# Kernel tuning notes

Hardware: AMD Instinct MI355X
Metric: run time of the kernel (lower is better)

## Reference

```python
import jax, jax.numpy as jnp
import numpy as np

B, C, H, W = 4, 256, 64, 64
C8 = C // 8  # q/k projection dim = 32

def setup_inputs() -> dict:
    key = jax.random.key(0)
    ks = jax.random.split(key, 6)
    s = 0.02
    return {
        "x": jax.random.normal(ks[0], (B, C, H, W), dtype=jnp.float32),
        "wq": jax.random.normal(ks[1], (C8, C), dtype=jnp.float32) * s,
        "bq": jnp.zeros((C8,), dtype=jnp.float32),
        "wk": jax.random.normal(ks[2], (C8, C), dtype=jnp.float32) * s,
        "bk": jnp.zeros((C8,), dtype=jnp.float32),
        "wv": jax.random.normal(ks[3], (C, C), dtype=jnp.float32) * s,
        "bv": jnp.zeros((C,), dtype=jnp.float32),
        "wo": jax.random.normal(ks[4], (C, C), dtype=jnp.float32) * s,
        "bo": jnp.zeros((C,), dtype=jnp.float32),
        "scale": jnp.zeros((1,), dtype=jnp.float32),
    }

def reference(x, wq, bq, wk, bk, wv, bv, wo, bo, scale):
    b, c, h, w = x.shape
    n = h * w
    xf = x.reshape(b, c, n)  # (B, C, N)
    # 1x1 convs are channel-mixing GEMMs
    q = jnp.einsum('oc,bcn->bon', wq, xf) + bq[None, :, None]  # (B, C8, N)
    k = jnp.einsum('oc,bcn->bon', wk, xf) + bk[None, :, None]  # (B, C8, N)
    v = jnp.einsum('oc,bcn->bon', wv, xf) + bv[None, :, None]  # (B, C,  N)
    inv_sqrt = 1.0 / jnp.sqrt(jnp.asarray(c // 8, dtype=x.dtype))
    scores = jnp.einsum('bon,bom->bnm', q, k) * inv_sqrt  # (B, N, N): query n, key m
    attn = jax.nn.softmax(scores, axis=-1)
    # torch: bmm(value, attn^T) -> attended[:, :, n] = sum_m v[:, :, m] * attn[n, m]
    attended = jnp.einsum('bcm,bnm->bcn', v, attn)  # (B, C, N)
    out = jnp.einsum('oc,bcn->bon', wo, attended) + bo[None, :, None]
    out = out.reshape(b, c, h, w)
    return x + scale[0] * out
```

## Files before the change

### kernel.cpp

```cpp
#include <hip/hip_runtime.h>
#include <stdint.h>

#define B_ 4
#define C_ 256
#define C8_ 32
#define N_ 4096
#define LOG2E 1.4426950408889634f
#define INV_SQRT32 0.17677669529663689f
#define QSCALE (INV_SQRT32 * LOG2E)

typedef __bf16 bf16x8 __attribute__((ext_vector_type(8)));
typedef float f32x16 __attribute__((ext_vector_type(16)));
typedef unsigned int uint4v __attribute__((ext_vector_type(4)));

__device__ __forceinline__ uint16_t f2bf(float f) {
  uint32_t u = __builtin_bit_cast(uint32_t, f);
  return (uint16_t)((u + 0x7FFFu + ((u >> 16) & 1u)) >> 16);
}
__device__ __forceinline__ uint32_t pack2bf(float a, float b) {
  uint32_t ua = __builtin_bit_cast(uint32_t, a);
  uint32_t ub = __builtin_bit_cast(uint32_t, b);
  ua = (ua + 0x7FFFu + ((ua >> 16) & 1u)) >> 16;
  ub = (ub + 0x7FFFu + ((ub >> 16) & 1u)) & 0xFFFF0000u;
  return ua | ub;
}
__device__ __forceinline__ bf16x8 load_bf8(const uint16_t* p) {
  uint4v u = *(const uint4v*)p;
  return __builtin_bit_cast(bf16x8, u);
}
__device__ __forceinline__ f32x16 mfma32(bf16x8 a, bf16x8 b, f32x16 c) {
  return __builtin_amdgcn_mfma_f32_32x32x16_bf16(a, b, c, 0, 0, 0);
}
__device__ __forceinline__ f32x16 mfma32_f8(long a, long b, f32x16 c) {
  return __builtin_amdgcn_mfma_f32_32x32x16_fp8_fp8(a, b, c, 0, 0, 0);
}
__device__ __forceinline__ long u2l(uint2 u) {
  return (long)(((uint64_t)u.y << 32) | u.x);
}

__global__ void k_wcast(const float* __restrict__ wq, const float* __restrict__ wk,
                        const float* __restrict__ wv, const float* __restrict__ wo,
                        uint16_t* __restrict__ wqb, uint16_t* __restrict__ wkb,
                        uint16_t* __restrict__ wvb, uint16_t* __restrict__ wob) {
  int i = blockIdx.x * 256 + threadIdx.x;
  if (i < 8192) {
    int o = i >> 8, c = i & 255;
    wqb[((size_t)(c >> 3) * 32 + o) * 8 + (c & 7)] = f2bf(wq[i]);
  } else if (i < 16384) {
    int j = i - 8192; int o = j >> 8, c = j & 255;
    wkb[((size_t)(c >> 3) * 32 + o) * 8 + (c & 7)] = f2bf(wk[j]);
  } else if (i < 81920) {
    int j = i - 16384; int o = j >> 8, c = j & 255;
    wvb[((size_t)(c >> 3) * 256 + o) * 8 + (c & 7)] = f2bf(wv[j]);
  } else {
    int j = i - 81920; int o = j >> 8, c = j & 255;
    wob[((size_t)(c >> 3) * 256 + o) * 8 + (c & 7)] = f2bf(wo[j]);
  }
}

__global__ __launch_bounds__(640) void k_proj_qkv(
    const float* __restrict__ x,
    const uint16_t* __restrict__ wqb, const float* __restrict__ bq,
    const uint16_t* __restrict__ wkb, const float* __restrict__ bk,
    const uint16_t* __restrict__ wvb, const float* __restrict__ bv,
    uint16_t* __restrict__ Qb, uint16_t* __restrict__ Kt, uint8_t* __restrict__ V8) {
  __shared__ uint4v xTv[32 * 32];
  int b = blockIdx.y;
  int n0 = blockIdx.x * 32;
  int tid = threadIdx.x;
  uint16_t* xT = (uint16_t*)xTv;

  if (tid < 256) {
    int r = tid >> 3;
    int l4 = (tid & 7) * 4;
#pragma unroll
    for (int p = 0; p < 8; p++) {
      int c = p * 32 + r;
      float4 v = *(const float4*)(x + ((size_t)b * C_ + c) * N_ + n0 + l4);
      int cg = c >> 3, cj = c & 7;
      xT[(cg * 32 + l4 + 0) * 8 + cj] = f2bf(v.x);
      xT[(cg * 32 + l4 + 1) * 8 + cj] = f2bf(v.y);
      xT[(cg * 32 + l4 + 2) * 8 + cj] = f2bf(v.z);
      xT[(cg * 32 + l4 + 3) * 8 + cj] = f2bf(v.w);
    }
  }
  __syncthreads();

  int wave = tid >> 6;
  int lane = tid & 63;
  int h = lane >> 5, ln = lane & 31;

  if (wave == 0) {
    f32x16 aq;
#pragma unroll
    for (int i = 0; i < 16; i++) aq[i] = 0.0f;
#pragma unroll 4
    for (int c = 0; c < C_; c += 16) {
      bf16x8 bb = __builtin_bit_cast(bf16x8, xTv[(c / 8 + h) * 32 + ln]);
      aq = mfma32(load_bf8(wqb + ((size_t)(c / 8 + h) * 32 + ln) * 8), bb, aq);
    }
#pragma unroll
    for (int g = 0; g < 4; g++) {
      int row = g * 8 + h * 4;
      uint2 pq;
      pq.x = pack2bf((aq[4 * g + 0] + bq[row + 0]) * QSCALE,
                     (aq[4 * g + 1] + bq[row + 1]) * QSCALE);
      pq.y = pack2bf((aq[4 * g + 2] + bq[row + 2]) * QSCALE,
                     (aq[4 * g + 3] + bq[row + 3]) * QSCALE);
      *(uint2*)(Qb + ((size_t)b * N_ + n0 + ln) * C8_ + row) = pq;
    }
  } else if (wave == 1) {
    f32x16 ak;
#pragma unroll
    for (int i = 0; i < 16; i++) ak[i] = 0.0f;
#pragma unroll 4
    for (int c = 0; c < C_; c += 16) {
      bf16x8 bb = __builtin_bit_cast(bf16x8, xTv[(c / 8 + h) * 32 + ln]);
      ak = mfma32(load_bf8(wkb + ((size_t)(c / 8 + h) * 32 + ln) * 8), bb, ak);
    }
#pragma unroll
    for (int g = 0; g < 4; g++) {
      int row = g * 8 + h * 4;
      uint2 pk;
      pk.x = pack2bf(ak[4 * g + 0] + bk[row + 0], ak[4 * g + 1] + bk[row + 1]);
      pk.y = pack2bf(ak[4 * g + 2] + bk[row + 2], ak[4 * g + 3] + bk[row + 3]);
      *(uint2*)(Kt + ((size_t)(b * 4 + g) * N_ + n0 + ln) * 8 + h * 4) = pk;
    }
  } else {
    int o0 = (wave - 2) * 32;
    f32x16 a0;
#pragma unroll
    for (int i = 0; i < 16; i++) a0[i] = 0.0f;
#pragma unroll 4
    for (int c = 0; c < C_; c += 16) {
      bf16x8 xa = __builtin_bit_cast(bf16x8, xTv[(c / 8 + h) * 32 + ln]);
      a0 = mfma32(xa, load_bf8(wvb + ((size_t)(c / 8 + h) * 256 + o0 + ln) * 8), a0);
    }
    int och = o0 + ln;
    float b0v = bv[och];
    size_t kgb = (size_t)(b * 512 + (n0 >> 3));
#pragma unroll
    for (int g = 0; g < 4; ++g) {
      uint32_t w0 = __builtin_amdgcn_cvt_pk_fp8_f32(a0[4 * g + 0] + b0v,
                                                    a0[4 * g + 1] + b0v, 0, false);
      w0 = __builtin_amdgcn_cvt_pk_fp8_f32(a0[4 * g + 2] + b0v,
                                           a0[4 * g + 3] + b0v, w0, true);
      *(uint32_t*)(V8 + ((kgb + g) * 256 + och) * 8 + 4 * h) = w0;
    }
  }
}

__global__ __launch_bounds__(512, 4) void k_attn(
    const uint16_t* __restrict__ Qb, const uint16_t* __restrict__ Kt,
    const uint8_t* __restrict__ V8, const uint16_t* __restrict__ Wob,
    const float* __restrict__ bo, const float* __restrict__ x,
    const float* __restrict__ scale, float* __restrict__ out) {
  __shared__ uint32_t Pl[2][2048];
  __shared__ uint4v aTv[32 * 32];
  __shared__ float sl[8][32];

  int bx = blockIdx.x;
  int b = bx >> 1;
  int qt = blockIdx.y + 64 * (bx & 1);
  int wave = threadIdx.x >> 6;
  int lane = threadIdx.x & 63;
  int h = lane >> 5, ln = lane & 31;
  int qi = qt * 32 + ln;

  const uint16_t* qrow = Qb + ((size_t)b * N_ + qi) * C8_;
  bf16x8 qf1 = load_bf8(qrow + h * 8);
  bf16x8 qf2 = load_bf8(qrow + 16 + h * 8);
  const uint16_t* k1base = Kt + ((size_t)(b * 4 + h) * N_) * 8;
  const uint16_t* k2base = Kt + ((size_t)(b * 4 + 2 + h) * N_) * 8;

  int o0 = wave * 32;
  const uint8_t* vbase =
      V8 + (size_t)(b * 512) * 2048 + (size_t)h * 2048 + (size_t)(o0 + ln) * 8;

  f32x16 O;
#pragma unroll
  for (int r = 0; r < 16; r++) O[r] = 0.0f;
  float lsum = 0.0f;

  const int K0 = wave * 32;
  bf16x8 ka1 = load_bf8(k1base + (size_t)(K0 + ln) * 8);
  bf16x8 ka2 = load_bf8(k2base + (size_t)(K0 + ln) * 8);

  for (int c = 0; c < 16; ++c) {
    int kbn = ((c + 1) & 15) * 256 + K0;
    bf16x8 kn1 = load_bf8(k1base + (size_t)(kbn + ln) * 8);
    bf16x8 kn2 = load_bf8(k2base + (size_t)(kbn + ln) * 8);

    f32x16 S;
#pragma unroll
    for (int i = 0; i < 16; i++) S[i] = 0.0f;
    S = mfma32(ka1, qf1, S);
    S = mfma32(ka2, qf2, S);

    float P[16];
#pragma unroll
    for (int r = 0; r < 16; r++) P[r] = __builtin_amdgcn_exp2f(fminf(S[r], 7.5f));
    float l0 = 0.0f, l1 = 0.0f;
#pragma unroll
    for (int r = 0; r < 8; r++) { l0 += P[r]; l1 += P[r + 8]; }
    lsum += l0 + l1;

    uint32_t w0 = __builtin_amdgcn_cvt_pk_fp8_f32(P[0], P[1], 0, false);
    w0 = __builtin_amdgcn_cvt_pk_fp8_f32(P[2], P[3], w0, true);
    uint32_t w1 = __builtin_amdgcn_cvt_pk_fp8_f32(P[4], P[5], 0, false);
    w1 = __builtin_amdgcn_cvt_pk_fp8_f32(P[6], P[7], w1, true);
    uint32_t w2 = __builtin_amdgcn_cvt_pk_fp8_f32(P[8], P[9], 0, false);
    w2 = __builtin_amdgcn_cvt_pk_fp8_f32(P[10], P[11], w2, true);
    uint32_t w3 = __builtin_amdgcn_cvt_pk_fp8_f32(P[12], P[13], 0, false);
    w3 = __builtin_amdgcn_cvt_pk_fp8_f32(P[14], P[15], w3, true);
    uint32_t* pw = &Pl[c & 1][wave * 256 + ln * 2 + h];
    pw[0] = w0; pw[64] = w1; pw[128] = w2; pw[192] = w3;

    __syncthreads();

    const uint8_t* vp = vbase + (size_t)c * 65536;
    const uint32_t* pb = &Pl[c & 1][h * 64 + ln * 2];
    __builtin_amdgcn_s_setprio(1);
#pragma unroll 4
    for (int g = 0; g < 16; ++g) {
      uint2 u1 = *(const uint2*)(vp + (size_t)g * 4096);
      uint2 pu = *(const uint2*)(pb + g * 128);
      O = mfma32_f8(u2l(u1), u2l(pu), O);
    }
    __builtin_amdgcn_s_setprio(0);
    ka1 = kn1; ka2 = kn2;
  }

  lsum += __shfl_xor(lsum, 32, 64);
  if (h == 0) sl[wave][ln] = lsum;
  __syncthreads();
  float lg = 0.0f;
#pragma unroll
  for (int w = 0; w < 8; w++) lg += sl[w][ln];
  float inv = 1.0f / lg;
  uint2* aT2 = (uint2*)aTv;
#pragma unroll
  for (int g = 0; g < 4; ++g) {
    uint2 pr2;
    pr2.x = pack2bf(O[4 * g + 0] * inv, O[4 * g + 1] * inv);
    pr2.y = pack2bf(O[4 * g + 2] * inv, O[4 * g + 3] * inv);
    aT2[((wave * 4 + g) * 32 + ln) * 2 + h] = pr2;
  }
  __syncthreads();

  f32x16 acc;
#pragma unroll
  for (int i = 0; i < 16; i++) acc[i] = 0.0f;
#pragma unroll 4
  for (int cc = 0; cc < C_; cc += 16) {
    bf16x8 a = load_bf8(Wob + ((size_t)(cc / 8 + h) * 256 + o0 + ln) * 8);
    bf16x8 bb = __builtin_bit_cast(bf16x8, aTv[(cc / 8 + h) * 32 + ln]);
    acc = mfma32(a, bb, acc);
  }
  float s = scale[0];
#pragma unroll
  for (int r = 0; r < 16; r++) {
    int row = (r & 3) + 8 * (r >> 2) + 4 * h;
    int o = o0 + row;
    size_t idx = ((size_t)b * C_ + o) * N_ + qi;
    out[idx] = x[idx] + s * (acc[r] + bo[o]);
  }
}

extern "C" void kernel_launch(void* const* d_in, const int* in_sizes, int n_in,
                              void* d_out, int out_size, void* d_ws, size_t ws_size,
                              hipStream_t stream) {
  const float* x  = (const float*)d_in[0];
  const float* wq = (const float*)d_in[1];
  const float* bq = (const float*)d_in[2];
  const float* wk = (const float*)d_in[3];
  const float* bk = (const float*)d_in[4];
  const float* wv = (const float*)d_in[5];
  const float* bv = (const float*)d_in[6];
  const float* wo = (const float*)d_in[7];
  const float* bo = (const float*)d_in[8];
  const float* scale = (const float*)d_in[9];
  float* out = (float*)d_out;

  char* w = (char*)d_ws;
  uint16_t* Qb  = (uint16_t*)(w);
  uint16_t* Kt  = (uint16_t*)(w + (1u << 20));
  uint8_t*  V8  = (uint8_t*)(w + (2u << 20));
  uint16_t* Wqb = (uint16_t*)(w + (6u << 20));
  uint16_t* Wkb = Wqb + 32 * 256;
  uint16_t* Wvb = Wkb + 32 * 256;
  uint16_t* Wob = Wvb + 256 * 256;

  k_wcast<<<576, 256, 0, stream>>>(wq, wk, wv, wo, Wqb, Wkb, Wvb, Wob);
  k_proj_qkv<<<dim3(N_ / 32, B_), 640, 0, stream>>>(x, Wqb, bq, Wkb, bk, Wvb, bv,
                                                    Qb, Kt, V8);
  k_attn<<<dim3(8, 64), 512, 0, stream>>>(Qb, Kt, V8, Wob, bo, x, scale, out);
}
```

Before: 143.8 us.

## Process two query tiles per block and software-pipeline P production with PV MFMA

Each attention block now handles 64 queries as two 32-query tiles, so every fp8 V fragment loaded from global memory feeds two MFMAs and K loads are shared across both tiles. This halves V/K global traffic per query. The loop is also restructured so that the exp/convert of chunk c overlaps the PV MFMA of chunk c-1, which leaves one barrier per iteration. In exchange, register use roughly doubles (launch bounds drop to 2 waves/SIMD), the grid halves to 256 blocks, and LDS use grows.

```diff
diff --git a/kernel.cpp b/kernel.cpp
--- a/kernel.cpp
+++ b/kernel.cpp
@@ -36,6 +36,22 @@
 }
 __device__ __forceinline__ long u2l(uint2 u) {
   return (long)(((uint64_t)u.y << 32) | u.x);
+}
+
+__device__ __forceinline__ float produce_P(const f32x16 S, uint32_t* pw) {
+  float P[16];
+#pragma unroll
+  for (int r = 0; r < 16; r++) P[r] = __builtin_amdgcn_exp2f(fminf(S[r], 7.5f));
+  float l0 = 0.0f, l1 = 0.0f;
+#pragma unroll
+  for (int r = 0; r < 8; r++) { l0 += P[r]; l1 += P[r + 8]; }
+#pragma unroll
+  for (int s = 0; s < 4; ++s) {
+    uint32_t w = __builtin_amdgcn_cvt_pk_fp8_f32(P[4 * s + 0], P[4 * s + 1], 0, false);
+    w = __builtin_amdgcn_cvt_pk_fp8_f32(P[4 * s + 2], P[4 * s + 3], w, true);
+    pw[s * 64] = w;
+  }
+  return l0 + l1;
 }
 
 __global__ void k_wcast(const float* __restrict__ wq, const float* __restrict__ wk,
@@ -150,26 +166,30 @@
   }
 }
 
-__global__ __launch_bounds__(512, 4) void k_attn(
+__global__ __launch_bounds__(512, 2) void k_attn(
     const uint16_t* __restrict__ Qb, const uint16_t* __restrict__ Kt,
     const uint8_t* __restrict__ V8, const uint16_t* __restrict__ Wob,
     const float* __restrict__ bo, const float* __restrict__ x,
     const float* __restrict__ scale, float* __restrict__ out) {
-  __shared__ uint32_t Pl[2][2048];
-  __shared__ uint4v aTv[32 * 32];
-  __shared__ float sl[8][32];
+  __shared__ uint32_t Pl[2][2][2048];
+  __shared__ uint4v aTv[32 * 64];
+  __shared__ float sl[8][2][32];
 
   int bx = blockIdx.x;
   int b = bx >> 1;
-  int qt = blockIdx.y + 64 * (bx & 1);
+  int qt = blockIdx.y + 32 * (bx & 1);
   int wave = threadIdx.x >> 6;
   int lane = threadIdx.x & 63;
   int h = lane >> 5, ln = lane & 31;
-  int qi = qt * 32 + ln;
-
-  const uint16_t* qrow = Qb + ((size_t)b * N_ + qi) * C8_;
-  bf16x8 qf1 = load_bf8(qrow + h * 8);
-  bf16x8 qf2 = load_bf8(qrow + 16 + h * 8);
+  int qiA = qt * 64 + ln;
+  int qiB = qiA + 32;
+
+  const uint16_t* qrowA = Qb + ((size_t)b * N_ + qiA) * C8_;
+  const uint16_t* qrowB = Qb + ((size_t)b * N_ + qiB) * C8_;
+  bf16x8 qf1A = load_bf8(qrowA + h * 8);
+  bf16x8 qf2A = load_bf8(qrowA + 16 + h * 8);
+  bf16x8 qf1B = load_bf8(qrowB + h * 8);
+  bf16x8 qf2B = load_bf8(qrowB + 16 + h * 8);
   const uint16_t* k1base = Kt + ((size_t)(b * 4 + h) * N_) * 8;
   const uint16_t* k2base = Kt + ((size_t)(b * 4 + 2 + h) * N_) * 8;
 
@@ -177,93 +197,124 @@
   const uint8_t* vbase =
       V8 + (size_t)(b * 512) * 2048 + (size_t)h * 2048 + (size_t)(o0 + ln) * 8;
 
-  f32x16 O;
-#pragma unroll
-  for (int r = 0; r < 16; r++) O[r] = 0.0f;
-  float lsum = 0.0f;
+  f32x16 OA, OB;
+#pragma unroll
+  for (int r = 0; r < 16; r++) { OA[r] = 0.0f; OB[r] = 0.0f; }
+  float lsA = 0.0f, lsB = 0.0f;
 
   const int K0 = wave * 32;
   bf16x8 ka1 = load_bf8(k1base + (size_t)(K0 + ln) * 8);
   bf16x8 ka2 = load_bf8(k2base + (size_t)(K0 + ln) * 8);
 
-  for (int c = 0; c < 16; ++c) {
+  {
+    bf16x8 kn1 = load_bf8(k1base + (size_t)(256 + K0 + ln) * 8);
+    bf16x8 kn2 = load_bf8(k2base + (size_t)(256 + K0 + ln) * 8);
+    f32x16 SA, SB;
+#pragma unroll
+    for (int i = 0; i < 16; i++) { SA[i] = 0.0f; SB[i] = 0.0f; }
+    SA = mfma32(ka1, qf1A, SA);
+    SA = mfma32(ka2, qf2A, SA);
+    SB = mfma32(ka1, qf1B, SB);
+    SB = mfma32(ka2, qf2B, SB);
+    lsA += produce_P(SA, &Pl[0][0][wave * 256 + ln * 2 + h]);
+    lsB += produce_P(SB, &Pl[0][1][wave * 256 + ln * 2 + h]);
+    ka1 = kn1; ka2 = kn2;
+  }
+  __syncthreads();
+
+  for (int c = 1; c < 16; ++c) {
     int kbn = ((c + 1) & 15) * 256 + K0;
     bf16x8 kn1 = load_bf8(k1base + (size_t)(kbn + ln) * 8);
     bf16x8 kn2 = load_bf8(k2base + (size_t)(kbn + ln) * 8);
 
-    f32x16 S;
-#pragma unroll
-    for (int i = 0; i < 16; i++) S[i] = 0.0f;
-    S = mfma32(ka1, qf1, S);
-    S = mfma32(ka2, qf2, S);
-
-    float P[16];
-#pragma unroll
-    for (int r = 0; r < 16; r++) P[r] = __builtin_amdgcn_exp2f(fminf(S[r], 7.5f));
-    float l0 = 0.0f, l1 = 0.0f;
-#pragma unroll
-    for (int r = 0; r < 8; r++) { l0 += P[r]; l1 += P[r + 8]; }
-    lsum += l0 + l1;
-
-    uint32_t w0 = __builtin_amdgcn_cvt_pk_fp8_f32(P[0], P[1], 0, false);
-    w0 = __builtin_amdgcn_cvt_pk_fp8_f32(P[2], P[3], w0, true);
-    uint32_t w1 = __builtin_amdgcn_cvt_pk_fp8_f32(P[4], P[5], 0, false);
-    w1 = __builtin_amdgcn_cvt_pk_fp8_f32(P[6], P[7], w1, true);
-    uint32_t w2 = __builtin_amdgcn_cvt_pk_fp8_f32(P[8], P[9], 0, false);
-    w2 = __builtin_amdgcn_cvt_pk_fp8_f32(P[10], P[11], w2, true);
-    uint32_t w3 = __builtin_amdgcn_cvt_pk_fp8_f32(P[12], P[13], 0, false);
-    w3 = __builtin_amdgcn_cvt_pk_fp8_f32(P[14], P[15], w3, true);
-    uint32_t* pw = &Pl[c & 1][wave * 256 + ln * 2 + h];
-    pw[0] = w0; pw[64] = w1; pw[128] = w2; pw[192] = w3;
-
-    __syncthreads();
-
-    const uint8_t* vp = vbase + (size_t)c * 65536;
-    const uint32_t* pb = &Pl[c & 1][h * 64 + ln * 2];
+    f32x16 SA, SB;
+#pragma unroll
+    for (int i = 0; i < 16; i++) { SA[i] = 0.0f; SB[i] = 0.0f; }
+    SA = mfma32(ka1, qf1A, SA);
+    SA = mfma32(ka2, qf2A, SA);
+    SB = mfma32(ka1, qf1B, SB);
+    SB = mfma32(ka2, qf2B, SB);
+
+    const uint8_t* vp = vbase + (size_t)(c - 1) * 65536;
+    const uint32_t* pbA = &Pl[(c - 1) & 1][0][h * 64 + ln * 2];
+    const uint32_t* pbB = &Pl[(c - 1) & 1][1][h * 64 + ln * 2];
     __builtin_amdgcn_s_setprio(1);
 #pragma unroll 4
     for (int g = 0; g < 16; ++g) {
       uint2 u1 = *(const uint2*)(vp + (size_t)g * 4096);
-      uint2 pu = *(const uint2*)(pb + g * 128);
-      O = mfma32_f8(u2l(u1), u2l(pu), O);
+      long v = u2l(u1);
+      uint2 puA = *(const uint2*)(pbA + g * 128);
+      uint2 puB = *(const uint2*)(pbB + g * 128);
+      OA = mfma32_f8(v, u2l(puA), OA);
+      OB = mfma32_f8(v, u2l(puB), OB);
     }
     __builtin_amdgcn_s_setprio(0);
+
+    lsA += produce_P(SA, &Pl[c & 1][0][wave * 256 + ln * 2 + h]);
+    lsB += produce_P(SB, &Pl[c & 1][1][wave * 256 + ln * 2 + h]);
+
+    __syncthreads();
     ka1 = kn1; ka2 = kn2;
   }
 
-  lsum += __shfl_xor(lsum, 32, 64);
-  if (h == 0) sl[wave][ln] = lsum;
+  {
+    const uint8_t* vp = vbase + (size_t)15 * 65536;
+    const uint32_t* pbA = &Pl[1][0][h * 64 + ln * 2];
+    const uint32_t* pbB = &Pl[1][1][h * 64 + ln * 2];
+    __builtin_amdgcn_s_setprio(1);
+#pragma unroll 4
+    for (int g = 0; g < 16; ++g) {
+      uint2 u1 = *(const uint2*)(vp + (size_t)g * 4096);
+      long v = u2l(u1);
+      uint2 puA = *(const uint2*)(pbA + g * 128);
+      uint2 puB = *(const uint2*)(pbB + g * 128);
+      OA = mfma32_f8(v, u2l(puA), OA);
+      OB = mfma32_f8(v, u2l(puB), OB);
+    }
+    __builtin_amdgcn_s_setprio(0);
+  }
+
+  lsA += __shfl_xor(lsA, 32, 64);
+  lsB += __shfl_xor(lsB, 32, 64);
+  if (h == 0) { sl[wave][0][ln] = lsA; sl[wave][1][ln] = lsB; }
   __syncthreads();
-  float lg = 0.0f;
-#pragma unroll
-  for (int w = 0; w < 8; w++) lg += sl[w][ln];
-  float inv = 1.0f / lg;
+  float lgA = 0.0f, lgB = 0.0f;
+#pragma unroll
+  for (int w = 0; w < 8; w++) { lgA += sl[w][0][ln]; lgB += sl[w][1][ln]; }
+  float invA = 1.0f / lgA, invB = 1.0f / lgB;
   uint2* aT2 = (uint2*)aTv;
 #pragma unroll
   for (int g = 0; g < 4; ++g) {
-    uint2 pr2;
-    pr2.x = pack2bf(O[4 * g + 0] * inv, O[4 * g + 1] * inv);
-    pr2.y = pack2bf(O[4 * g + 2] * inv, O[4 * g + 3] * inv);
-    aT2[((wave * 4 + g) * 32 + ln) * 2 + h] = pr2;
+    uint2 prA, prB;
+    prA.x = pack2bf(OA[4 * g + 0] * invA, OA[4 * g + 1] * invA);
+    prA.y = pack2bf(OA[4 * g + 2] * invA, OA[4 * g + 3] * invA);
+    aT2[(((wave * 4 + g) * 64) + ln) * 2 + h] = prA;
+    prB.x = pack2bf(OB[4 * g + 0] * invB, OB[4 * g + 1] * invB);
+    prB.y = pack2bf(OB[4 * g + 2] * invB, OB[4 * g + 3] * invB);
+    aT2[(((wave * 4 + g) * 64) + 32 + ln) * 2 + h] = prB;
   }
   __syncthreads();
 
-  f32x16 acc;
-#pragma unroll
-  for (int i = 0; i < 16; i++) acc[i] = 0.0f;
+  f32x16 accA, accB;
+#pragma unroll
+  for (int i = 0; i < 16; i++) { accA[i] = 0.0f; accB[i] = 0.0f; }
 #pragma unroll 4
   for (int cc = 0; cc < C_; cc += 16) {
     bf16x8 a = load_bf8(Wob + ((size_t)(cc / 8 + h) * 256 + o0 + ln) * 8);
-    bf16x8 bb = __builtin_bit_cast(bf16x8, aTv[(cc / 8 + h) * 32 + ln]);
-    acc = mfma32(a, bb, acc);
+    bf16x8 bbA = __builtin_bit_cast(bf16x8, aTv[(cc / 8 + h) * 64 + ln]);
+    bf16x8 bbB = __builtin_bit_cast(bf16x8, aTv[(cc / 8 + h) * 64 + 32 + ln]);
+    accA = mfma32(a, bbA, accA);
+    accB = mfma32(a, bbB, accB);
   }
   float s = scale[0];
 #pragma unroll
   for (int r = 0; r < 16; r++) {
     int row = (r & 3) + 8 * (r >> 2) + 4 * h;
     int o = o0 + row;
-    size_t idx = ((size_t)b * C_ + o) * N_ + qi;
-    out[idx] = x[idx] + s * (acc[r] + bo[o]);
+    size_t idxA = ((size_t)b * C_ + o) * N_ + qiA;
+    size_t idxB = idxA + 32;
+    out[idxA] = x[idxA] + s * (accA[r] + bo[o]);
+    out[idxB] = x[idxB] + s * (accB[r] + bo[o]);
   }
 }
 
@@ -294,5 +345,5 @@
   k_wcast<<<576, 256, 0, stream>>>(wq, wk, wv, wo, Wqb, Wkb, Wvb, Wob);
   k_proj_qkv<<<dim3(N_ / 32, B_), 640, 0, stream>>>(x, Wqb, bq, Wkb, bk, Wvb, bv,
                                                     Qb, Kt, V8);
-  k_attn<<<dim3(8, 64), 512, 0, stream>>>(Qb, Kt, V8, Wob, bo, x, scale, out);
-}
+  k_attn<<<dim3(8, 32), 512, 0, stream>>>(Qb, Kt, V8, Wob, bo, x, scale, out);
+}
```

After: 183.9 us. 1.28x slower.

## Fuse weight bf16 casting into projection kernels and drop separate cast kernel

Applied to the files above, without the earlier changes.

Removes the standalone weight-cast kernel and has the projection and output GEMMs read fp32 weights directly, converting them to bf16 in registers. This saves one kernel launch and a round trip of the cast weights through global memory. In exchange, every block repeats the conversion and reads twice as many weight bytes. The x-tile transpose load is also spread over 512 threads instead of 256.

```diff
diff --git a/kernel.cpp b/kernel.cpp
--- a/kernel.cpp
+++ b/kernel.cpp
@@ -28,6 +28,16 @@
   uint4v u = *(const uint4v*)p;
   return __builtin_bit_cast(bf16x8, u);
 }
+__device__ __forceinline__ bf16x8 load_f32_bf8(const float* p) {
+  float4 a = *(const float4*)p;
+  float4 b = *(const float4*)(p + 4);
+  uint4v u;
+  u.x = pack2bf(a.x, a.y);
+  u.y = pack2bf(a.z, a.w);
+  u.z = pack2bf(b.x, b.y);
+  u.w = pack2bf(b.z, b.w);
+  return __builtin_bit_cast(bf16x8, u);
+}
 __device__ __forceinline__ f32x16 mfma32(bf16x8 a, bf16x8 b, f32x16 c) {
   return __builtin_amdgcn_mfma_f32_32x32x16_bf16(a, b, c, 0, 0, 0);
 }
@@ -38,31 +48,11 @@
   return (long)(((uint64_t)u.y << 32) | u.x);
 }
 
-__global__ void k_wcast(const float* __restrict__ wq, const float* __restrict__ wk,
-                        const float* __restrict__ wv, const float* __restrict__ wo,
-                        uint16_t* __restrict__ wqb, uint16_t* __restrict__ wkb,
-                        uint16_t* __restrict__ wvb, uint16_t* __restrict__ wob) {
-  int i = blockIdx.x * 256 + threadIdx.x;
-  if (i < 8192) {
-    int o = i >> 8, c = i & 255;
-    wqb[((size_t)(c >> 3) * 32 + o) * 8 + (c & 7)] = f2bf(wq[i]);
-  } else if (i < 16384) {
-    int j = i - 8192; int o = j >> 8, c = j & 255;
-    wkb[((size_t)(c >> 3) * 32 + o) * 8 + (c & 7)] = f2bf(wk[j]);
-  } else if (i < 81920) {
-    int j = i - 16384; int o = j >> 8, c = j & 255;
-    wvb[((size_t)(c >> 3) * 256 + o) * 8 + (c & 7)] = f2bf(wv[j]);
-  } else {
-    int j = i - 81920; int o = j >> 8, c = j & 255;
-    wob[((size_t)(c >> 3) * 256 + o) * 8 + (c & 7)] = f2bf(wo[j]);
-  }
-}
-
 __global__ __launch_bounds__(640) void k_proj_qkv(
     const float* __restrict__ x,
-    const uint16_t* __restrict__ wqb, const float* __restrict__ bq,
-    const uint16_t* __restrict__ wkb, const float* __restrict__ bk,
-    const uint16_t* __restrict__ wvb, const float* __restrict__ bv,
+    const float* __restrict__ wq, const float* __restrict__ bq,
+    const float* __restrict__ wk, const float* __restrict__ bk,
+    const float* __restrict__ wv, const float* __restrict__ bv,
     uint16_t* __restrict__ Qb, uint16_t* __restrict__ Kt, uint8_t* __restrict__ V8) {
   __shared__ uint4v xTv[32 * 32];
   int b = blockIdx.y;
@@ -70,11 +60,13 @@
   int tid = threadIdx.x;
   uint16_t* xT = (uint16_t*)xTv;
 
-  if (tid < 256) {
-    int r = tid >> 3;
+  if (tid < 512) {
+    int r = tid >> 4;
+    int ph = (tid >> 3) & 1;
     int l4 = (tid & 7) * 4;
 #pragma unroll
-    for (int p = 0; p < 8; p++) {
+    for (int pp = 0; pp < 4; pp++) {
+      int p = pp * 2 + ph;
       int c = p * 32 + r;
       float4 v = *(const float4*)(x + ((size_t)b * C_ + c) * N_ + n0 + l4);
       int cg = c >> 3, cj = c & 7;
@@ -94,10 +86,11 @@
     f32x16 aq;
 #pragma unroll
     for (int i = 0; i < 16; i++) aq[i] = 0.0f;
+    const float* wrow = wq + (size_t)ln * C_ + h * 8;
 #pragma unroll 4
     for (int c = 0; c < C_; c += 16) {
       bf16x8 bb = __builtin_bit_cast(bf16x8, xTv[(c / 8 + h) * 32 + ln]);
-      aq = mfma32(load_bf8(wqb + ((size_t)(c / 8 + h) * 32 + ln) * 8), bb, aq);
+      aq = mfma32(load_f32_bf8(wrow + c), bb, aq);
     }
 #pragma unroll
     for (int g = 0; g < 4; g++) {
@@ -113,10 +106,11 @@
     f32x16 ak;
 #pragma unroll
     for (int i = 0; i < 16; i++) ak[i] = 0.0f;
+    const float* wrow = wk + (size_t)ln * C_ + h * 8;
 #pragma unroll 4
     for (int c = 0; c < C_; c += 16) {
       bf16x8 bb = __builtin_bit_cast(bf16x8, xTv[(c / 8 + h) * 32 + ln]);
-      ak = mfma32(load_bf8(wkb + ((size_t)(c / 8 + h) * 32 + ln) * 8), bb, ak);
+      ak = mfma32(load_f32_bf8(wrow + c), bb, ak);
     }
 #pragma unroll
     for (int g = 0; g < 4; g++) {
@@ -128,15 +122,16 @@
     }
   } else {
     int o0 = (wave - 2) * 32;
+    int och = o0 + ln;
     f32x16 a0;
 #pragma unroll
     for (int i = 0; i < 16; i++) a0[i] = 0.0f;
+    const float* wrow = wv + (size_t)och * C_ + h * 8;
 #pragma unroll 4
     for (int c = 0; c < C_; c += 16) {
       bf16x8 xa = __builtin_bit_cast(bf16x8, xTv[(c / 8 + h) * 32 + ln]);
-      a0 = mfma32(xa, load_bf8(wvb + ((size_t)(c / 8 + h) * 256 + o0 + ln) * 8), a0);
-    }
-    int och = o0 + ln;
+      a0 = mfma32(xa, load_f32_bf8(wrow + c), a0);
+    }
     float b0v = bv[och];
     size_t kgb = (size_t)(b * 512 + (n0 >> 3));
 #pragma unroll
@@ -152,7 +147,7 @@
 
 __global__ __launch_bounds__(512, 4) void k_attn(
     const uint16_t* __restrict__ Qb, const uint16_t* __restrict__ Kt,
-    const uint8_t* __restrict__ V8, const uint16_t* __restrict__ Wob,
+    const uint8_t* __restrict__ V8, const float* __restrict__ wo,
     const float* __restrict__ bo, const float* __restrict__ x,
     const float* __restrict__ scale, float* __restrict__ out) {
   __shared__ uint32_t Pl[2][2048];
@@ -251,9 +246,10 @@
   f32x16 acc;
 #pragma unroll
   for (int i = 0; i < 16; i++) acc[i] = 0.0f;
+  const float* worow = wo + (size_t)(o0 + ln) * C_ + h * 8;
 #pragma unroll 4
   for (int cc = 0; cc < C_; cc += 16) {
-    bf16x8 a = load_bf8(Wob + ((size_t)(cc / 8 + h) * 256 + o0 + ln) * 8);
+    bf16x8 a = load_f32_bf8(worow + cc);
     bf16x8 bb = __builtin_bit_cast(bf16x8, aTv[(cc / 8 + h) * 32 + ln]);
     acc = mfma32(a, bb, acc);
   }
@@ -286,13 +282,8 @@
   uint16_t* Qb  = (uint16_t*)(w);
   uint16_t* Kt  = (uint16_t*)(w + (1u << 20));
   uint8_t*  V8  = (uint8_t*)(w + (2u << 20));
-  uint16_t* Wqb = (uint16_t*)(w + (6u << 20));
-  uint16_t* Wkb = Wqb + 32 * 256;
-  uint16_t* Wvb = Wkb + 32 * 256;
-  uint16_t* Wob = Wvb + 256 * 256;
-
-  k_wcast<<<576, 256, 0, stream>>>(wq, wk, wv, wo, Wqb, Wkb, Wvb, Wob);
-  k_proj_qkv<<<dim3(N_ / 32, B_), 640, 0, stream>>>(x, Wqb, bq, Wkb, bk, Wvb, bv,
+
+  k_proj_qkv<<<dim3(N_ / 32, B_), 640, 0, stream>>>(x, wq, bq, wk, bk, wv, bv,
                                                     Qb, Kt, V8);
-  k_attn<<<dim3(8, 64), 512, 0, stream>>>(Qb, Kt, V8, Wob, bo, x, scale, out);
-}
+  k_attn<<<dim3(8, 64), 512, 0, stream>>>(Qb, Kt, V8, wo, bo, x, scale, out);
+}
```

Measured after the change: 163.4 us. 13.6% more time.
